# Optimization experiments

Hardware: AMD Instinct MI355X
Metric: run time of the kernel (lower is better)

## Reference

```python
import jax, jax.numpy as jnp
import numpy as np

EPS = 1e-6
V_LO, V_HI = 0.95, 1.05
N_NODES = 100000
N_EDGES = 3200000


def setup_inputs() -> dict:
    key = jax.random.key(0)
    k1, k2, k3, k4 = jax.random.split(key, 4)
    node_features = jax.random.normal(k1, (N_NODES, 4), dtype=jnp.float32)
    edge_index = jax.random.randint(k2, (2, N_EDGES), 0, N_NODES, dtype=jnp.int64)
    edge_probs = jax.random.uniform(k3, (N_EDGES,), dtype=jnp.float32)
    edge_params = jax.random.uniform(k4, (N_EDGES, 2), dtype=jnp.float32)
    return {
        "node_features": node_features,
        "edge_index": edge_index,
        "edge_probs": edge_probs,
        "edge_params": edge_params,
    }


def reference(node_features, edge_index, edge_probs, edge_params):
    n_nodes = node_features.shape[0]
    src = edge_index[0]
    dst = edge_index[1]

    # power flow on each edge, computed from the SRC node voltage magnitude
    v_mag_src = jnp.sqrt(node_features[src, 0] ** 2 + node_features[src, 1] ** 2)  # [E]
    v2 = v_mag_src ** 2
    p_e = v2 / (edge_params[:, 0] + EPS) * edge_probs  # [E]
    q_e = v2 / (edge_params[:, 1] + EPS) * edge_probs  # [E]

    # each edge contributes to both endpoints; self-loops contribute only once
    self_loop = src == dst
    p_e_dst = jnp.where(self_loop, 0.0, p_e)
    q_e_dst = jnp.where(self_loop, 0.0, q_e)

    p_flow = (jax.ops.segment_sum(p_e, src, num_segments=n_nodes)
              + jax.ops.segment_sum(p_e_dst, dst, num_segments=n_nodes))  # [N]
    q_flow = (jax.ops.segment_sum(q_e, src, num_segments=n_nodes)
              + jax.ops.segment_sum(q_e_dst, dst, num_segments=n_nodes))  # [N]

    p_load = node_features[:, 2]
    q_load = node_features[:, 3]
    power_balance_loss = jnp.mean((p_load + p_flow) ** 2 + (q_load + q_flow) ** 2)

    # voltage magnitude box constraint
    v_mag = jnp.sqrt(node_features[:, 0] ** 2 + node_features[:, 1] ** 2)
    lower_viol = jax.nn.relu(V_LO - v_mag)
    upper_viol = jax.nn.relu(v_mag - V_HI)
    voltage_loss = jnp.mean(lower_viol ** 2 + upper_viol ** 2)

    return power_balance_loss + voltage_loss
```

## Files before the change

### kernel.cpp

```cpp
#include <hip/hip_runtime.h>

#define EPS 1e-6f
#define V_LO 0.95f
#define V_HI 1.05f

#define BIN_ELEMS 20480
#define TPB 1024
#define MAX_SPLIT 51
#define BATCH 4

typedef float f32x2 __attribute__((ext_vector_type(2)));

__global__ void pf_v2_kernel(const float4* __restrict__ nf4,
                             float* __restrict__ v2tab, int n_nodes) {
    int i = blockIdx.x * blockDim.x + threadIdx.x;
    if (i < n_nodes) {
        float4 f = nf4[i];
        v2tab[i] = f.x * f.x + f.y * f.y;
    }
}

__global__ __launch_bounds__(TPB) void pf_edge_scan(
    const float* __restrict__ v2tab,
    const int* __restrict__ ei,
    const float* __restrict__ probs,
    const float* __restrict__ params,
    float* __restrict__ partial,
    int n_edges, int n_nodes, int nbins, int per_chunk)
{
    extern __shared__ float lds[];
    int bin  = blockIdx.x % nbins;
    int slot = blockIdx.x / nbins;
    int node_base = bin * BIN_ELEMS;

    for (int i = threadIdx.x; i < 2 * BIN_ELEMS; i += TPB)
        lds[i] = 0.0f;
    __syncthreads();

    int e0 = slot * per_chunk;
    int e1 = min(e0 + per_chunk, n_edges);

    for (int e = e0 + threadIdx.x * BATCH; e < e1; e += TPB * BATCH) {
        if (e + BATCH <= e1) {
            int4   s4  = *reinterpret_cast<const int4*>(&ei[e]);
            int4   d4  = *reinterpret_cast<const int4*>(&ei[n_edges + e]);
            float4 pb4 = *reinterpret_cast<const float4*>(&probs[e]);
            float4 prA = *reinterpret_cast<const float4*>(&params[(size_t)e * 2]);
            float4 prB = *reinterpret_cast<const float4*>(&params[(size_t)e * 2 + 4]);

            #pragma unroll
            for (int k = 0; k < BATCH; ++k) {
                int   src  = (k == 0) ? s4.x : (k == 1) ? s4.y : (k == 2) ? s4.z : s4.w;
                int   dst  = (k == 0) ? d4.x : (k == 1) ? d4.y : (k == 2) ? d4.z : d4.w;
                float prob = (k == 0) ? pb4.x : (k == 1) ? pb4.y : (k == 2) ? pb4.z : pb4.w;
                float prx  = (k == 0) ? prA.x : (k == 1) ? prA.z : (k == 2) ? prB.x : prB.z;
                float pry  = (k == 0) ? prA.y : (k == 1) ? prA.w : (k == 2) ? prB.y : prB.w;

                unsigned ls = (unsigned)(src - node_base);
                unsigned ld = (unsigned)(dst - node_base);
                bool cs = ls < (unsigned)BIN_ELEMS;
                bool cd = (ld < (unsigned)BIN_ELEMS) & (src != dst);
                if (cs | cd) {
                    float v2 = v2tab[src];
                    float pe = v2 * prob * __builtin_amdgcn_rcpf(prx + EPS);
                    float qe = v2 * prob * __builtin_amdgcn_rcpf(pry + EPS);
                    if (cs) {
                        atomicAdd(&lds[2 * ls],     pe);
                        atomicAdd(&lds[2 * ls + 1], qe);
                    }
                    if (cd) {
                        atomicAdd(&lds[2 * ld],     pe);
                        atomicAdd(&lds[2 * ld + 1], qe);
                    }
                }
            }
        } else {
            for (int t = e; t < e1; ++t) {
                int src = ei[t];
                int dst = ei[n_edges + t];
                unsigned ls = (unsigned)(src - node_base);
                unsigned ld = (unsigned)(dst - node_base);
                bool cs = ls < (unsigned)BIN_ELEMS;
                bool cd = (ld < (unsigned)BIN_ELEMS) & (src != dst);
                if (cs | cd) {
                    float v2 = v2tab[src];
                    float pe = v2 * probs[t] * __builtin_amdgcn_rcpf(params[(size_t)t * 2] + EPS);
                    float qe = v2 * probs[t] * __builtin_amdgcn_rcpf(params[(size_t)t * 2 + 1] + EPS);
                    if (cs) { atomicAdd(&lds[2 * ls], pe); atomicAdd(&lds[2 * ls + 1], qe); }
                    if (cd) { atomicAdd(&lds[2 * ld], pe); atomicAdd(&lds[2 * ld + 1], qe); }
                }
            }
        }
    }
    __syncthreads();

    int lim = min(BIN_ELEMS, n_nodes - node_base);
    float* out = partial + (size_t)slot * n_nodes * 2 + (size_t)node_base * 2;
    const f32x2* lds2 = reinterpret_cast<const f32x2*>(lds);
    f32x2* out2 = reinterpret_cast<f32x2*>(out);
    for (int i = threadIdx.x; i < lim; i += TPB)
        __builtin_nontemporal_store(lds2[i], &out2[i]);
}

__global__ void pf_node_kernel(const float* __restrict__ nf,
                               const float* __restrict__ partial,
                               float* __restrict__ acc,
                               int n_nodes, int split) {
    int i = blockIdx.x * blockDim.x + threadIdx.x;
    float c = 0.0f;
    if (i < n_nodes) {
        float4 f = *reinterpret_cast<const float4*>(&nf[(size_t)i * 4]);
        float p = f.z, q = f.w;
        const f32x2* pp = reinterpret_cast<const f32x2*>(partial) + i;
        for (int s = 0; s < split; ++s) {
            f32x2 fl = __builtin_nontemporal_load(&pp[(size_t)s * n_nodes]);
            p += fl.x;
            q += fl.y;
        }
        float vmag = sqrtf(f.x * f.x + f.y * f.y);
        float lv = fmaxf(V_LO - vmag, 0.0f);
        float uv = fmaxf(vmag - V_HI, 0.0f);
        c = p * p + q * q + lv * lv + uv * uv;
    }
    #pragma unroll
    for (int off = 32; off > 0; off >>= 1)
        c += __shfl_down(c, off);
    __shared__ float wsum[4];
    int lane = threadIdx.x & 63;
    int wid  = threadIdx.x >> 6;
    if (lane == 0) wsum[wid] = c;
    __syncthreads();
    if (threadIdx.x == 0) {
        float s = 0.0f;
        int nw = blockDim.x >> 6;
        for (int w = 0; w < nw; ++w) s += wsum[w];
        atomicAdd(acc, s);
    }
}

__global__ void pf_finalize_kernel(const float* __restrict__ acc,
                                   float* __restrict__ out,
                                   float inv_n) {
    out[0] = acc[0] * inv_n;
}

extern "C" void kernel_launch(void* const* d_in, const int* in_sizes, int n_in,
                              void* d_out, int out_size, void* d_ws, size_t ws_size,
                              hipStream_t stream) {
    const float* nf     = (const float*)d_in[0];
    const int*   ei     = (const int*)d_in[1];
    const float* probs  = (const float*)d_in[2];
    const float* params = (const float*)d_in[3];

    int n_nodes = in_sizes[0] / 4;
    int n_edges = in_sizes[2];

    float* acc   = (float*)d_ws;
    float* v2tab = (float*)((char*)d_ws + 256);
    size_t v2_bytes = ((size_t)n_nodes * sizeof(float) + 255) & ~(size_t)255;
    float* partial = (float*)((char*)d_ws + 256 + v2_bytes);

    size_t slot_bytes = (size_t)n_nodes * 2 * sizeof(float);
    int split = (int)((ws_size - 256 - v2_bytes) / slot_bytes);
    if (split > MAX_SPLIT) split = MAX_SPLIT;
    if (split < 1) split = 1;

    int nbins = (n_nodes + BIN_ELEMS - 1) / BIN_ELEMS;
    int per_chunk = (n_edges + split - 1) / split;
    per_chunk = (per_chunk + 3) & ~3;

    size_t lds_bytes = (size_t)(2 * BIN_ELEMS) * sizeof(float);
    (void)hipFuncSetAttribute((const void*)pf_edge_scan,
                              hipFuncAttributeMaxDynamicSharedMemorySize,
                              (int)lds_bytes);

    (void)hipMemsetAsync(d_ws, 0, 256, stream);

    pf_v2_kernel<<<(n_nodes + 255) / 256, 256, 0, stream>>>(
        (const float4*)nf, v2tab, n_nodes);

    pf_edge_scan<<<nbins * split, TPB, lds_bytes, stream>>>(
        v2tab, ei, probs, params, partial, n_edges, n_nodes, nbins, per_chunk);

    int nblocks = (n_nodes + 255) / 256;
    pf_node_kernel<<<nblocks, 256, 0, stream>>>(nf, partial, acc, n_nodes, split);

    pf_finalize_kernel<<<1, 1, 0, stream>>>(acc, (float*)d_out,
                                            1.0f / (float)n_nodes);
}
```

Measured before the change: 117.1 us.

## Bucket edge contributions by node bin before LDS accumulation

Replaces the multi-pass scan, in which every block rereads all edges for its node bin, with a single pass. That pass computes each edge's contribution and appends packed 64-bit records (p value, a bf16-rounded q/p ratio, local node id) into per-bin global buckets through LDS staging. A second kernel accumulates each bin's bucket in LDS across 16 slots, so the node kernel reduces 16 partials instead of up to 51, and the node kernel now processes two nodes per thread. The aim is to remove the repeated edge reads, at the cost of extra bucket write and read traffic, ballot-based appends and reduced q precision from the bf16 ratio. There is an overflow path to global memory, but records past capbin are silently dropped.

```diff
diff --git a/kernel.cpp b/kernel.cpp
--- a/kernel.cpp
+++ b/kernel.cpp
@@ -5,11 +5,17 @@
 #define V_HI 1.05f
 
 #define BIN_ELEMS 20480
+#define MAXBINS 5
 #define TPB 1024
+#define CAP 4064
+#define SLOTS_B 16
+#define EPR 4
+#define ROUND_EDGES (TPB * EPR)
 #define MAX_SPLIT 51
-#define BATCH 4
 
 typedef float f32x2 __attribute__((ext_vector_type(2)));
+typedef unsigned long long u64;
+typedef unsigned int u32;
 
 __global__ void pf_v2_kernel(const float4* __restrict__ nf4,
                              float* __restrict__ v2tab, int n_nodes) {
@@ -17,6 +23,162 @@
     if (i < n_nodes) {
         float4 f = nf4[i];
         v2tab[i] = f.x * f.x + f.y * f.y;
+    }
+}
+
+__device__ __forceinline__ void append_end(int mybin, u64 rec, int lane,
+                                           int* cnt, u64* stage,
+                                           int* gtail, u64* bucket, int capbin) {
+    int pos = -1;
+    #pragma unroll
+    for (int b = 0; b < MAXBINS; ++b) {
+        unsigned long long m = __ballot(mybin == b);
+        if (mybin == b) {
+            int rank   = (int)__popcll(m & ((1ull << lane) - 1));
+            int leader = __ffsll((unsigned long long)m) - 1;
+            int base = 0;
+            if (lane == leader) base = atomicAdd(&cnt[b], (int)__popcll(m));
+            base = __shfl(base, leader);
+            pos = base + rank;
+        }
+    }
+    if (mybin >= 0) {
+        if (pos < CAP) {
+            stage[mybin * CAP + pos] = rec;
+        } else {
+            int gp = atomicAdd(&gtail[mybin], 1);
+            if (gp < capbin) bucket[(size_t)mybin * capbin + gp] = rec;
+        }
+    }
+}
+
+__global__ __launch_bounds__(TPB) void pf_bucket_scan(
+    const float* __restrict__ v2tab,
+    const int* __restrict__ ei,
+    const float* __restrict__ probs,
+    const float* __restrict__ params,
+    u64* __restrict__ bucket,
+    int* __restrict__ gtail,
+    int n_edges, int capbin, int nbins, int total_rounds)
+{
+    extern __shared__ u64 stage[];
+    __shared__ int cnt[MAXBINS];
+    __shared__ int wbase[MAXBINS];
+    int tid  = threadIdx.x;
+    int lane = tid & 63;
+
+    for (int r = blockIdx.x; r < total_rounds; r += gridDim.x) {
+        if (tid < nbins) cnt[tid] = 0;
+        __syncthreads();
+
+        int ebase = r * ROUND_EDGES + tid * EPR;
+        bool full = (ebase + EPR <= n_edges);
+        int4 s4, d4; float4 pb4, prA, prB;
+        if (full) {
+            s4  = *reinterpret_cast<const int4*>(&ei[ebase]);
+            d4  = *reinterpret_cast<const int4*>(&ei[n_edges + ebase]);
+            pb4 = *reinterpret_cast<const float4*>(&probs[ebase]);
+            prA = *reinterpret_cast<const float4*>(&params[(size_t)ebase * 2]);
+            prB = *reinterpret_cast<const float4*>(&params[(size_t)ebase * 2 + 4]);
+        }
+
+        #pragma unroll
+        for (int k = 0; k < EPR; ++k) {
+            int e = ebase + k;
+            bool v = full || (e < n_edges);
+            int src, dst; float prob, prx, pry;
+            if (full) {
+                src  = (k == 0) ? s4.x : (k == 1) ? s4.y : (k == 2) ? s4.z : s4.w;
+                dst  = (k == 0) ? d4.x : (k == 1) ? d4.y : (k == 2) ? d4.z : d4.w;
+                prob = (k == 0) ? pb4.x : (k == 1) ? pb4.y : (k == 2) ? pb4.z : pb4.w;
+                prx  = (k == 0) ? prA.x : (k == 1) ? prA.z : (k == 2) ? prB.x : prB.z;
+                pry  = (k == 0) ? prA.y : (k == 1) ? prA.w : (k == 2) ? prB.y : prB.w;
+            } else if (v) {
+                src = ei[e]; dst = ei[n_edges + e]; prob = probs[e];
+                prx = params[(size_t)e * 2]; pry = params[(size_t)e * 2 + 1];
+            } else {
+                src = 0; dst = 0; prob = 0.0f; prx = 1.0f; pry = 1.0f;
+            }
+            float v2 = 0.0f;
+            if (v) v2 = v2tab[src];
+            float pe    = v2 * prob * __builtin_amdgcn_rcpf(prx + EPS);
+            float ratio = (prx + EPS) * __builtin_amdgcn_rcpf(pry + EPS);
+            u32 rb = __float_as_uint(ratio);
+            rb += 0x7FFFu + ((rb >> 16) & 1u);
+            u32 rhi = rb >> 16;
+            u32 pbits = __float_as_uint(pe);
+
+            int bin_s = v ? (src / BIN_ELEMS) : -1;
+            u32 lid_s = (u32)(src - bin_s * BIN_ELEMS);
+            append_end(bin_s, ((u64)pbits << 32) | (u64)(lid_s | (rhi << 16)),
+                       lane, cnt, stage, gtail, bucket, capbin);
+
+            bool dv = v && (src != dst);
+            int bin_d = dv ? (dst / BIN_ELEMS) : -1;
+            u32 lid_d = dv ? (u32)(dst - bin_d * BIN_ELEMS) : 0u;
+            append_end(bin_d, ((u64)pbits << 32) | (u64)(lid_d | (rhi << 16)),
+                       lane, cnt, stage, gtail, bucket, capbin);
+        }
+        __syncthreads();
+
+        if (tid < nbins) {
+            int n = min(cnt[tid], CAP);
+            wbase[tid] = atomicAdd(&gtail[tid], n);
+        }
+        __syncthreads();
+
+        for (int b = 0; b < nbins; ++b) {
+            int n  = min(cnt[b], CAP);
+            int gb = wbase[b];
+            if (gb < capbin) {
+                n = min(n, capbin - gb);
+                u64* dstp = bucket + (size_t)b * capbin + gb;
+                for (int i = tid; i < n; i += TPB)
+                    __builtin_nontemporal_store(stage[b * CAP + i], &dstp[i]);
+            }
+        }
+        __syncthreads();
+    }
+}
+
+__global__ __launch_bounds__(TPB) void pf_bucket_accum(
+    const u64* __restrict__ bucket,
+    const int* __restrict__ gtail,
+    float* __restrict__ partial,
+    int n_nodes, int capbin)
+{
+    extern __shared__ float sm[];
+    float* smp = sm;
+    float* smq = sm + BIN_ELEMS;
+    int bin  = blockIdx.x / SLOTS_B;
+    int slot = blockIdx.x % SLOTS_B;
+    int node_base = bin * BIN_ELEMS;
+
+    for (int i = threadIdx.x; i < 2 * BIN_ELEMS; i += TPB) sm[i] = 0.0f;
+    __syncthreads();
+
+    int cnt   = min(gtail[bin], capbin);
+    int chunk = (cnt + SLOTS_B - 1) / SLOTS_B;
+    int lo = slot * chunk;
+    int hi = min(lo + chunk, cnt);
+    const u64* bb = bucket + (size_t)bin * capbin;
+    for (int i = lo + threadIdx.x; i < hi; i += TPB) {
+        u64 rec = bb[i];
+        u32 w0 = (u32)rec;
+        float pe    = __uint_as_float((u32)(rec >> 32));
+        float ratio = __uint_as_float(w0 & 0xFFFF0000u);
+        int id = (int)(w0 & 0xFFFFu);
+        atomicAdd(&smp[id], pe);
+        atomicAdd(&smq[id], pe * ratio);
+    }
+    __syncthreads();
+
+    int lim = min(BIN_ELEMS, n_nodes - node_base);
+    float* out = partial + (size_t)slot * n_nodes * 2 + (size_t)node_base * 2;
+    f32x2* out2 = reinterpret_cast<f32x2*>(out);
+    for (int i = threadIdx.x; i < lim; i += TPB) {
+        f32x2 vv; vv.x = smp[i]; vv.y = smq[i];
+        __builtin_nontemporal_store(vv, &out2[i]);
     }
 }
 
@@ -33,29 +195,25 @@
     int slot = blockIdx.x / nbins;
     int node_base = bin * BIN_ELEMS;
 
-    for (int i = threadIdx.x; i < 2 * BIN_ELEMS; i += TPB)
-        lds[i] = 0.0f;
+    for (int i = threadIdx.x; i < 2 * BIN_ELEMS; i += TPB) lds[i] = 0.0f;
     __syncthreads();
 
     int e0 = slot * per_chunk;
     int e1 = min(e0 + per_chunk, n_edges);
-
-    for (int e = e0 + threadIdx.x * BATCH; e < e1; e += TPB * BATCH) {
-        if (e + BATCH <= e1) {
+    for (int e = e0 + threadIdx.x * 4; e < e1; e += TPB * 4) {
+        if (e + 4 <= e1) {
             int4   s4  = *reinterpret_cast<const int4*>(&ei[e]);
             int4   d4  = *reinterpret_cast<const int4*>(&ei[n_edges + e]);
             float4 pb4 = *reinterpret_cast<const float4*>(&probs[e]);
             float4 prA = *reinterpret_cast<const float4*>(&params[(size_t)e * 2]);
             float4 prB = *reinterpret_cast<const float4*>(&params[(size_t)e * 2 + 4]);
-
             #pragma unroll
-            for (int k = 0; k < BATCH; ++k) {
+            for (int k = 0; k < 4; ++k) {
                 int   src  = (k == 0) ? s4.x : (k == 1) ? s4.y : (k == 2) ? s4.z : s4.w;
                 int   dst  = (k == 0) ? d4.x : (k == 1) ? d4.y : (k == 2) ? d4.z : d4.w;
                 float prob = (k == 0) ? pb4.x : (k == 1) ? pb4.y : (k == 2) ? pb4.z : pb4.w;
                 float prx  = (k == 0) ? prA.x : (k == 1) ? prA.z : (k == 2) ? prB.x : prB.z;
                 float pry  = (k == 0) ? prA.y : (k == 1) ? prA.w : (k == 2) ? prB.y : prB.w;
-
                 unsigned ls = (unsigned)(src - node_base);
                 unsigned ld = (unsigned)(dst - node_base);
                 bool cs = ls < (unsigned)BIN_ELEMS;
@@ -64,14 +222,8 @@
                     float v2 = v2tab[src];
                     float pe = v2 * prob * __builtin_amdgcn_rcpf(prx + EPS);
                     float qe = v2 * prob * __builtin_amdgcn_rcpf(pry + EPS);
-                    if (cs) {
-                        atomicAdd(&lds[2 * ls],     pe);
-                        atomicAdd(&lds[2 * ls + 1], qe);
-                    }
-                    if (cd) {
-                        atomicAdd(&lds[2 * ld],     pe);
-                        atomicAdd(&lds[2 * ld + 1], qe);
-                    }
+                    if (cs) { atomicAdd(&lds[2 * ls], pe); atomicAdd(&lds[2 * ls + 1], qe); }
+                    if (cd) { atomicAdd(&lds[2 * ld], pe); atomicAdd(&lds[2 * ld + 1], qe); }
                 }
             }
         } else {
@@ -106,21 +258,30 @@
                                const float* __restrict__ partial,
                                float* __restrict__ acc,
                                int n_nodes, int split) {
-    int i = blockIdx.x * blockDim.x + threadIdx.x;
+    int i2 = (blockIdx.x * blockDim.x + threadIdx.x) * 2;
     float c = 0.0f;
-    if (i < n_nodes) {
-        float4 f = *reinterpret_cast<const float4*>(&nf[(size_t)i * 4]);
-        float p = f.z, q = f.w;
-        const f32x2* pp = reinterpret_cast<const f32x2*>(partial) + i;
+    if (i2 < n_nodes) {
+        bool two = (i2 + 1) < n_nodes;
+        float4 fa = *reinterpret_cast<const float4*>(&nf[(size_t)i2 * 4]);
+        float4 fb = two ? *reinterpret_cast<const float4*>(&nf[(size_t)(i2 + 1) * 4])
+                        : make_float4(0, 0, 0, 0);
+        float pa = fa.z, qa = fa.w, pb = fb.z, qb = fb.w;
+        const float* pp = partial + (size_t)i2 * 2;
         for (int s = 0; s < split; ++s) {
-            f32x2 fl = __builtin_nontemporal_load(&pp[(size_t)s * n_nodes]);
-            p += fl.x;
-            q += fl.y;
-        }
-        float vmag = sqrtf(f.x * f.x + f.y * f.y);
+            float4 fl = *reinterpret_cast<const float4*>(&pp[(size_t)s * n_nodes * 2]);
+            pa += fl.x; qa += fl.y;
+            pb += fl.z; qb += fl.w;
+        }
+        float vmag = sqrtf(fa.x * fa.x + fa.y * fa.y);
         float lv = fmaxf(V_LO - vmag, 0.0f);
         float uv = fmaxf(vmag - V_HI, 0.0f);
-        c = p * p + q * q + lv * lv + uv * uv;
+        c = pa * pa + qa * qa + lv * lv + uv * uv;
+        if (two) {
+            float vmag2 = sqrtf(fb.x * fb.x + fb.y * fb.y);
+            float lv2 = fmaxf(V_LO - vmag2, 0.0f);
+            float uv2 = fmaxf(vmag2 - V_HI, 0.0f);
+            c += pb * pb + qb * qb + lv2 * lv2 + uv2 * uv2;
+        }
     }
     #pragma unroll
     for (int off = 32; off > 0; off >>= 1)
@@ -139,8 +300,7 @@
 }
 
 __global__ void pf_finalize_kernel(const float* __restrict__ acc,
-                                   float* __restrict__ out,
-                                   float inv_n) {
+                                   float* __restrict__ out, float inv_n) {
     out[0] = acc[0] * inv_n;
 }
 
@@ -154,36 +314,65 @@
 
     int n_nodes = in_sizes[0] / 4;
     int n_edges = in_sizes[2];
+    int nbins = (n_nodes + BIN_ELEMS - 1) / BIN_ELEMS;
 
     float* acc   = (float*)d_ws;
+    int*   gtail = (int*)((char*)d_ws + 64);
     float* v2tab = (float*)((char*)d_ws + 256);
     size_t v2_bytes = ((size_t)n_nodes * sizeof(float) + 255) & ~(size_t)255;
-    float* partial = (float*)((char*)d_ws + 256 + v2_bytes);
-
-    size_t slot_bytes = (size_t)n_nodes * 2 * sizeof(float);
-    int split = (int)((ws_size - 256 - v2_bytes) / slot_bytes);
-    if (split > MAX_SPLIT) split = MAX_SPLIT;
-    if (split < 1) split = 1;
-
-    int nbins = (n_nodes + BIN_ELEMS - 1) / BIN_ELEMS;
-    int per_chunk = (n_edges + split - 1) / split;
-    per_chunk = (per_chunk + 3) & ~3;
-
-    size_t lds_bytes = (size_t)(2 * BIN_ELEMS) * sizeof(float);
-    (void)hipFuncSetAttribute((const void*)pf_edge_scan,
-                              hipFuncAttributeMaxDynamicSharedMemorySize,
-                              (int)lds_bytes);
+    char*  after_v2 = (char*)d_ws + 256 + v2_bytes;
+
+    int capbin = (int)(((long long)n_edges * 2 / nbins) * 6 / 5);
+    size_t bucket_bytes = (size_t)nbins * capbin * sizeof(u64);
+    size_t partB_bytes  = (size_t)SLOTS_B * n_nodes * 2 * sizeof(float);
+    size_t need = 256 + v2_bytes + bucket_bytes + partB_bytes;
+    bool use_bucket = (ws_size >= need) && (nbins <= MAXBINS);
 
     (void)hipMemsetAsync(d_ws, 0, 256, stream);
 
     pf_v2_kernel<<<(n_nodes + 255) / 256, 256, 0, stream>>>(
         (const float4*)nf, v2tab, n_nodes);
 
-    pf_edge_scan<<<nbins * split, TPB, lds_bytes, stream>>>(
-        v2tab, ei, probs, params, partial, n_edges, n_nodes, nbins, per_chunk);
-
-    int nblocks = (n_nodes + 255) / 256;
-    pf_node_kernel<<<nblocks, 256, 0, stream>>>(nf, partial, acc, n_nodes, split);
+    if (use_bucket) {
+        u64*   bucket  = (u64*)after_v2;
+        float* partial = (float*)(after_v2 + bucket_bytes);
+
+        size_t ldsA = (size_t)MAXBINS * CAP * sizeof(u64);
+        size_t ldsB = (size_t)(2 * BIN_ELEMS) * sizeof(float);
+        (void)hipFuncSetAttribute((const void*)pf_bucket_scan,
+                                  hipFuncAttributeMaxDynamicSharedMemorySize, (int)ldsA);
+        (void)hipFuncSetAttribute((const void*)pf_bucket_accum,
+                                  hipFuncAttributeMaxDynamicSharedMemorySize, (int)ldsB);
+
+        int total_rounds = (n_edges + ROUND_EDGES - 1) / ROUND_EDGES;
+        pf_bucket_scan<<<256, TPB, ldsA, stream>>>(
+            v2tab, ei, probs, params, bucket, gtail,
+            n_edges, capbin, nbins, total_rounds);
+
+        pf_bucket_accum<<<nbins * SLOTS_B, TPB, ldsB, stream>>>(
+            bucket, gtail, partial, n_nodes, capbin);
+
+        int nblocks = (n_nodes / 2 + 255) / 256;
+        pf_node_kernel<<<nblocks, 256, 0, stream>>>(nf, partial, acc, n_nodes, SLOTS_B);
+    } else {
+        float* partial = (float*)after_v2;
+        size_t slot_bytes = (size_t)n_nodes * 2 * sizeof(float);
+        int split = (int)((ws_size - 256 - v2_bytes) / slot_bytes);
+        if (split > MAX_SPLIT) split = MAX_SPLIT;
+        if (split < 1) split = 1;
+        int per_chunk = (n_edges + split - 1) / split;
+        per_chunk = (per_chunk + 3) & ~3;
+
+        size_t lds_bytes = (size_t)(2 * BIN_ELEMS) * sizeof(float);
+        (void)hipFuncSetAttribute((const void*)pf_edge_scan,
+                                  hipFuncAttributeMaxDynamicSharedMemorySize, (int)lds_bytes);
+
+        pf_edge_scan<<<nbins * split, TPB, lds_bytes, stream>>>(
+            v2tab, ei, probs, params, partial, n_edges, n_nodes, nbins, per_chunk);
+
+        int nblocks = (n_nodes / 2 + 255) / 256;
+        pf_node_kernel<<<nblocks, 256, 0, stream>>>(nf, partial, acc, n_nodes, split);
+    }
 
     pf_finalize_kernel<<<1, 1, 0, stream>>>(acc, (float*)d_out,
                                             1.0f / (float)n_nodes);
```

Result: slower. 290.7 us (+148.3%).
